# Kernel tuning notes

Measured on AMD Instinct MI355X. Metric: run time of the kernel, lower is better.

The kernel has to match this reference:

```python
import jax, jax.numpy as jnp
import numpy as np

N_NODES = 50000
N_EDGES = 800000
IN_CH = 64
OUT_CH = 64


def setup_inputs() -> dict:
    key = jax.random.key(0)
    ks = jax.random.split(key, 20)
    inp = {
        'x': jax.random.normal(ks[0], (N_NODES, IN_CH), dtype=jnp.float32),
        'edge_index': jax.random.randint(ks[1], (2, N_EDGES), 0, N_NODES, dtype=jnp.int64),
        'edge_weight': jax.random.uniform(ks[2], (N_EDGES,), dtype=jnp.float32),
    }
    i = 3
    for g in ('z', 'r', 'h'):
        inp[f'Wx_{g}'] = 0.1 * jax.random.normal(ks[i], (2, IN_CH, OUT_CH), dtype=jnp.float32); i += 1
        inp[f'bx_{g}'] = 0.1 * jax.random.normal(ks[i], (OUT_CH,), dtype=jnp.float32); i += 1
        inp[f'Wh_{g}'] = 0.1 * jax.random.normal(ks[i], (2, OUT_CH, OUT_CH), dtype=jnp.float32); i += 1
        inp[f'bh_{g}'] = 0.1 * jax.random.normal(ks[i], (OUT_CH,), dtype=jnp.float32); i += 1
    inp['lin_W'] = 0.1 * jax.random.normal(ks[i], (OUT_CH, 1), dtype=jnp.float32); i += 1
    inp['lin_b'] = jnp.zeros((1,), dtype=jnp.float32)
    return inp


def _cheb_norm(edge_index, edge_weight, n_nodes):
    # sym-normalized scaled Laplacian with lambda_max=2: L_hat = -D^{-1/2} A D^{-1/2}
    src, dst = edge_index[0], edge_index[1]
    deg = jax.ops.segment_sum(edge_weight, src, num_segments=n_nodes)
    dinv = jnp.where(deg > 0, jax.lax.rsqrt(jnp.where(deg > 0, deg, 1.0)), 0.0)
    norm = -dinv[src] * edge_weight * dinv[dst]
    return src, dst, norm


def _cheb_conv(x, src, dst, norm, W, b, n_nodes):
    # K=2: out = x @ W0 + (L_hat x) @ W1 + b
    out = x @ W[0]
    tx1 = jax.ops.segment_sum(norm[:, None] * x[src], dst, num_segments=n_nodes)
    out = out + tx1 @ W[1]
    return out + b


def reference(x, edge_index, edge_weight,
              Wx_z, bx_z, Wh_z, bh_z,
              Wx_r, bx_r, Wh_r, bh_r,
              Wx_h, bx_h, Wh_h, bh_h,
              lin_W, lin_b):
    n = x.shape[0]
    src, dst, norm = _cheb_norm(edge_index, edge_weight, n)
    H = jnp.zeros((n, OUT_CH), dtype=x.dtype)  # GConvGRU initial hidden state
    Z = jax.nn.sigmoid(_cheb_conv(x, src, dst, norm, Wx_z, bx_z, n)
                       + _cheb_conv(H, src, dst, norm, Wh_z, bh_z, n))
    R = jax.nn.sigmoid(_cheb_conv(x, src, dst, norm, Wx_r, bx_r, n)
                       + _cheb_conv(H, src, dst, norm, Wh_r, bh_r, n))
    H_tilde = jnp.tanh(_cheb_conv(x, src, dst, norm, Wx_h, bx_h, n)
                       + _cheb_conv(H * R, src, dst, norm, Wh_h, bh_h, n))
    H = Z * H + (1.0 - Z) * H_tilde
    h = jax.nn.relu(H)
    return h @ lin_W + lin_b
```

## Files before the change

kernel.cpp:

```cpp
#include <hip/hip_runtime.h>
#include <hip/hip_bf16.h>

#define NN 50000
#define NE 800000
#define CH 64
#define NPW 8
#define NB 196
#define BCAPD 4608
#define BCAPS 4608
#define EPT 16
#define BIN_BLOCKS ((NE + 256*EPT - 1) / (256*EPT))

typedef __attribute__((ext_vector_type(4))) float f4;

#define OFF_TX1  0
#define OFF_BIND 0
#define OFF_BINS (NB*BCAPD*2)
#define OFF_DINV (NN*CH)
#define OFF_CNT  (OFF_DINV + NN)
#define OFF_GC   (OFF_CNT + NN)
#define OFF_BIAS (OFF_GC + 2*NB)
#define OFF_EREC (OFF_BIAS + 194)

__global__ void k_prep(const float* __restrict__ bxz, const float* __restrict__ bhz,
                       const float* __restrict__ bxh, const float* __restrict__ bhh,
                       const float* __restrict__ linW, const float* __restrict__ linb,
                       float* __restrict__ bias) {
    int i = threadIdx.x;
    bias[i]       = bxz[i] + bhz[i];
    bias[64 + i]  = bxh[i] + bhh[i];
    bias[128 + i] = linW[i];
    if (i == 0) bias[192] = linb[0];
}

__global__ __launch_bounds__(256) void k_bin(const int* __restrict__ ei,
                                             const float* __restrict__ ew,
                                             int2* __restrict__ binD,
                                             unsigned int* __restrict__ binS,
                                             int* __restrict__ gcD, int* __restrict__ gcS) {
    __shared__ int hD[NB], hS[NB], bD[NB], bS[NB];
    int t = threadIdx.x;
    for (int b = t; b < NB; b += 256) { hD[b] = 0; hS[b] = 0; }
    __syncthreads();

    int e0 = blockIdx.x * (256 * EPT);
    unsigned int sa[EPT];
    float wv[EPT];
    int sd[EPT], ss[EPT];
#pragma unroll
    for (int i = 0; i < EPT; i++) {
        int e = e0 + i * 256 + t;
        sd[i] = -1; ss[i] = -1; sa[i] = 0; wv[i] = 0.f;
        if (e < NE) {
            int s = ei[e];
            int d = ei[NE + e];
            wv[i] = ew[e];
            int bind = d >> 8;
            sa[i] = (unsigned int)s | ((unsigned int)(d & 255) << 16)
                  | ((unsigned int)bind << 24);
            sd[i] = atomicAdd(&hD[bind], 1);
            ss[i] = atomicAdd(&hS[s >> 8], 1);
        }
    }
    __syncthreads();
    for (int b = t; b < NB; b += 256) {
        bD[b] = atomicAdd(&gcD[b], hD[b]);
        bS[b] = atomicAdd(&gcS[b], hS[b]);
    }
    __syncthreads();
#pragma unroll
    for (int i = 0; i < EPT; i++) {
        if (sd[i] < 0) continue;
        unsigned int a = sa[i];
        int bind = a >> 24;
        int src  = a & 0xffff;
        int dlo  = (a >> 16) & 255;
        int pD = bD[bind] + sd[i];
        if (pD < BCAPD)
            binD[bind * BCAPD + pD] = make_int2((int)(a & 0xffffff), __float_as_int(wv[i]));
        int bins = src >> 8;
        int pS = bS[bins] + ss[i];
        if (pS < BCAPS)
            binS[bins * BCAPS + pS] = ((unsigned int)(src & 255) << 16)
                                    | ((__float_as_uint(wv[i]) + 0x8000u) >> 16);
    }
}

__global__ __launch_bounds__(1024) void k_bucket(const int2* __restrict__ binD,
                                                 const int* __restrict__ gcD,
                                                 unsigned int* __restrict__ erec, int cap,
                                                 int* __restrict__ cnt) {
    __shared__ int lcnt[256];
    int bin = blockIdx.x;
    int t = threadIdx.x;
    if (t < 256) lcnt[t] = 0;
    __syncthreads();
    int m = gcD[bin]; if (m > BCAPD) m = BCAPD;
    const int2* bp = binD + (size_t)bin * BCAPD;
    for (int j = t; j < m; j += 1024) {
        int2 r = bp[j];
        int dlo = (r.x >> 16) & 255;
        int src = r.x & 0xffff;
        int slot = atomicAdd(&lcnt[dlo], 1);
        if (slot < cap) {
            unsigned int wr = (__float_as_uint(__int_as_float(r.y)) + 0x8000u) >> 16;
            erec[(size_t)(bin * 256 + dlo) * cap + slot] = ((unsigned int)src << 16) | wr;
        }
    }
    __syncthreads();
    if (t < 256) {
        int idx = bin * 256 + t;
        if (idx < NN) cnt[idx] = lcnt[t];
    }
}

__global__ __launch_bounds__(1024) void k_deg(const unsigned int* __restrict__ binS,
                                              const int* __restrict__ gcS,
                                              float* __restrict__ dinv) {
    __shared__ float acc[256];
    int bin = blockIdx.x;
    int t = threadIdx.x;
    if (t < 256) acc[t] = 0.f;
    __syncthreads();
    int m = gcS[bin]; if (m > BCAPS) m = BCAPS;
    const unsigned int* bp = binS + (size_t)bin * BCAPS;
    for (int j = t; j < m; j += 1024) {
        unsigned int r = bp[j];
        float w = __uint_as_float((r & 0xffffu) << 16);
        atomicAdd(&acc[r >> 16], w);
    }
    __syncthreads();
    if (t < 256) {
        int idx = bin * 256 + t;
        if (idx < NN) {
            float d = acc[t];
            dinv[idx] = (d > 0.f) ? (1.f / sqrtf(d)) : 0.f;
        }
    }
}

__global__ __launch_bounds__(256) void k_gather(const float* __restrict__ x,
                                                const int* __restrict__ cnt,
                                                const float* __restrict__ dinv,
                                                const unsigned int* __restrict__ erec,
                                                int cap, float* __restrict__ tx1) {
    int w = (blockIdx.x * 256 + threadIdx.x) >> 6;
    if (w >= NN) return;
    int lane = threadIdx.x & 63;
    int g  = lane >> 4;
    int c4 = (lane & 15) * 4;
    int kn = cnt[w];
    if (kn > cap) kn = cap;
    const unsigned int* bp = erec + (size_t)w * cap;

    f4 t0 = {0.f, 0.f, 0.f, 0.f}, t1 = {0.f, 0.f, 0.f, 0.f};
    int j = 0;
    for (; j + 7 < kn; j += 8) {
        unsigned int r0 = bp[j + g];
        unsigned int r1 = bp[j + 4 + g];
        int s0 = r0 >> 16, s1 = r1 >> 16;
        float w0 = __uint_as_float((r0 & 0xffffu) << 16);
        float w1 = __uint_as_float((r1 & 0xffffu) << 16);
        float n0 = dinv[s0] * w0;
        float n1 = dinv[s1] * w1;
        const f4 x0 = *(const f4*)&x[(size_t)s0 * CH + c4];
        const f4 x1 = *(const f4*)&x[(size_t)s1 * CH + c4];
        t0 += n0 * x0;
        t1 += n1 * x1;
    }
    for (; j + 3 < kn; j += 4) {
        unsigned int r0 = bp[j + g];
        int s0 = r0 >> 16;
        float n0 = dinv[s0] * __uint_as_float((r0 & 0xffffu) << 16);
        const f4 x0 = *(const f4*)&x[(size_t)s0 * CH + c4];
        t0 += n0 * x0;
    }
    int rem = kn - j;
    if (g < rem) {
        unsigned int r = bp[j + g];
        int s0 = r >> 16;
        float n0 = dinv[s0] * __uint_as_float((r & 0xffffu) << 16);
        const f4 x0 = *(const f4*)&x[(size_t)s0 * CH + c4];
        t0 += n0 * x0;
    }
    f4 t = t0 + t1;
#pragma unroll
    for (int q = 0; q < 4; q++) {
        t[q] += __shfl_xor(t[q], 16);
        t[q] += __shfl_xor(t[q], 32);
    }
    if (g == 0) {
        f4 r = -dinv[w] * t;
        *(f4*)&tx1[(size_t)w * CH + c4] = r;
    }
}

__global__ __launch_bounds__(256) void k_node(const float* __restrict__ x,
                                              const float* __restrict__ tx1,
                                              const float* __restrict__ Wxz,
                                              const float* __restrict__ Wxh,
                                              const float* __restrict__ bias,
                                              float* __restrict__ out) {
    __shared__ float lds[4][NPW * 128];
    int wid  = threadIdx.x >> 6;
    int lane = threadIdx.x & 63;
    int base = (blockIdx.x * 4 + wid) * NPW;
    if (base >= NN) return;

    const float BZ  = bias[lane];
    const float BH  = bias[64 + lane];
    const float LWc = bias[128 + lane];
    const float LB  = bias[192];

    float* L = lds[wid];
#pragma unroll
    for (int n = 0; n < NPW; n++) {
        int node = base + n;
        if (node < NN) {
            L[n * 128 + lane]      = x[(size_t)node * CH + lane];
            L[n * 128 + 64 + lane] = tx1[(size_t)node * CH + lane];
        }
    }

    float az[NPW], ah[NPW];
#pragma unroll
    for (int n = 0; n < NPW; n++) { az[n] = BZ; ah[n] = BH; }

#pragma unroll 2
    for (int k = 0; k < CH; k += 4) {
        float wz0[4], wz1[4], wh0[4], wh1[4];
#pragma unroll
        for (int j = 0; j < 4; j++) {
            wz0[j] = Wxz[(k + j) * CH + lane];
            wz1[j] = Wxz[CH * CH + (k + j) * CH + lane];
            wh0[j] = Wxh[(k + j) * CH + lane];
            wh1[j] = Wxh[CH * CH + (k + j) * CH + lane];
        }
#pragma unroll
        for (int n = 0; n < NPW; n++) {
            const f4 xk = *(const f4*)&L[n * 128 + k];
            const f4 tk = *(const f4*)&L[n * 128 + 64 + k];
#pragma unroll
            for (int j = 0; j < 4; j++) {
                az[n] = fmaf(xk[j], wz0[j], az[n]);
                az[n] = fmaf(tk[j], wz1[j], az[n]);
                ah[n] = fmaf(xk[j], wh0[j], ah[n]);
                ah[n] = fmaf(tk[j], wh1[j], ah[n]);
            }
        }
    }

#pragma unroll
    for (int n = 0; n < NPW; n++) {
        float z  = 1.f / (1.f + expf(-az[n]));
        float ht = tanhf(ah[n]);
        float h  = (1.f - z) * ht;
        h = (h > 0.f) ? h : 0.f;
        float v = h * LWc;
#pragma unroll
        for (int off = 32; off > 0; off >>= 1) v += __shfl_xor(v, off);
        if (lane == 0 && base + n < NN) out[base + n] = v + LB;
    }
}

extern "C" void kernel_launch(void* const* d_in, const int* in_sizes, int n_in,
                              void* d_out, int out_size, void* d_ws, size_t ws_size,
                              hipStream_t stream) {
    const float* x   = (const float*)d_in[0];
    const int*   ei  = (const int*)d_in[1];
    const float* ew  = (const float*)d_in[2];
    const float* Wxz = (const float*)d_in[3];
    const float* bxz = (const float*)d_in[4];
    const float* bhz = (const float*)d_in[6];
    const float* Wxh = (const float*)d_in[11];
    const float* bxh = (const float*)d_in[12];
    const float* bhh = (const float*)d_in[14];
    const float* lW  = (const float*)d_in[15];
    const float* lb  = (const float*)d_in[16];
    float* ws  = (float*)d_ws;
    float* out = (float*)d_out;

    long long availInts = (long long)(ws_size / 4) - (long long)OFF_EREC;
    int cap = 64;
    if (availInts < (long long)NN * 64) cap = 48;
    if (availInts < (long long)NN * 48) cap = 32;
    unsigned int* erec = (unsigned int*)(ws + OFF_EREC);

    hipMemsetAsync(ws + OFF_GC, 0, 2 * NB * sizeof(int), stream);

    k_prep<<<1, 64, 0, stream>>>(bxz, bhz, bxh, bhh, lW, lb, ws + OFF_BIAS);
    k_bin<<<BIN_BLOCKS, 256, 0, stream>>>(ei, ew,
                                          (int2*)(ws + OFF_BIND),
                                          (unsigned int*)(ws + OFF_BINS),
                                          (int*)(ws + OFF_GC), (int*)(ws + OFF_GC) + NB);
    k_bucket<<<NB, 1024, 0, stream>>>((const int2*)(ws + OFF_BIND),
                                      (const int*)(ws + OFF_GC), erec, cap,
                                      (int*)(ws + OFF_CNT));
    k_deg<<<NB, 1024, 0, stream>>>((const unsigned int*)(ws + OFF_BINS),
                                   (const int*)(ws + OFF_GC) + NB, ws + OFF_DINV);
    k_gather<<<(NN * 64 + 255) / 256, 256, 0, stream>>>(x, (const int*)(ws + OFF_CNT),
                                                        ws + OFF_DINV, erec, cap,
                                                        ws + OFF_TX1);
    k_node<<<(NN + 4 * NPW - 1) / (4 * NPW), 256, 0, stream>>>(x, ws + OFF_TX1, Wxz, Wxh,
                                                               ws + OFF_BIAS, out);
}
```

Baseline: 121.3 us.

## Use bf16 MFMA for node GRU matmul with bf16 tx1 and pre-transposed weights

Measured after the change: 98.79 us. 1.23x faster.

```diff
diff --git a/kernel.cpp b/kernel.cpp
--- a/kernel.cpp
+++ b/kernel.cpp
@@ -4,7 +4,6 @@
 #define NN 50000
 #define NE 800000
 #define CH 64
-#define NPW 8
 #define NB 196
 #define BCAPD 4608
 #define BCAPS 4608
@@ -12,25 +11,47 @@
 #define BIN_BLOCKS ((NE + 256*EPT - 1) / (256*EPT))
 
 typedef __attribute__((ext_vector_type(4))) float f4;
+typedef __attribute__((ext_vector_type(4))) float f32x4;
+typedef __attribute__((ext_vector_type(8))) short bf16x8;
+typedef __attribute__((ext_vector_type(4))) unsigned int u32x4;
+typedef __attribute__((ext_vector_type(2))) unsigned int u32x2;
 
 #define OFF_TX1  0
 #define OFF_BIND 0
 #define OFF_BINS (NB*BCAPD*2)
-#define OFF_DINV (NN*CH)
+#define OFF_DINV (OFF_BINS + NB*BCAPS)
 #define OFF_CNT  (OFF_DINV + NN)
 #define OFF_GC   (OFF_CNT + NN)
 #define OFF_BIAS (OFF_GC + 2*NB)
-#define OFF_EREC (OFF_BIAS + 194)
-
-__global__ void k_prep(const float* __restrict__ bxz, const float* __restrict__ bhz,
-                       const float* __restrict__ bxh, const float* __restrict__ bhh,
+#define OFF_WT   (OFF_BIAS + 196)
+#define OFF_EREC (OFF_WT + 8192)
+
+__device__ __forceinline__ unsigned int bpack(float a, float b) {
+    return ((__float_as_uint(a) + 0x8000u) >> 16)
+         | ((__float_as_uint(b) + 0x8000u) & 0xffff0000u);
+}
+
+__global__ void k_prep(const float* __restrict__ Wxz, const float* __restrict__ bxz,
+                       const float* __restrict__ bhz,
+                       const float* __restrict__ Wxh, const float* __restrict__ bxh,
+                       const float* __restrict__ bhh,
                        const float* __restrict__ linW, const float* __restrict__ linb,
-                       float* __restrict__ bias) {
-    int i = threadIdx.x;
-    bias[i]       = bxz[i] + bhz[i];
-    bias[64 + i]  = bxh[i] + bhh[i];
-    bias[128 + i] = linW[i];
-    if (i == 0) bias[192] = linb[0];
+                       float* __restrict__ bias, unsigned short* __restrict__ wt) {
+    int idx = blockIdx.x * 256 + threadIdx.x;
+    if (idx < 2 * 64 * 128) {
+        int g = idx >> 13;
+        int c = (idx >> 7) & 63;
+        int k = idx & 127;
+        const float* W = g ? Wxh : Wxz;
+        float v = (k < 64) ? W[k * 64 + c] : W[4096 + (k - 64) * 64 + c];
+        wt[idx] = (unsigned short)((__float_as_uint(v) + 0x8000u) >> 16);
+    }
+    if (idx < 64) {
+        bias[idx]       = bxz[idx] + bhz[idx];
+        bias[64 + idx]  = bxh[idx] + bhh[idx];
+        bias[128 + idx] = linW[idx];
+    }
+    if (idx == 0) bias[192] = linb[0];
 }
 
 __global__ __launch_bounds__(256) void k_bin(const int* __restrict__ ei,
@@ -74,7 +95,6 @@
         unsigned int a = sa[i];
         int bind = a >> 24;
         int src  = a & 0xffff;
-        int dlo  = (a >> 16) & 255;
         int pD = bD[bind] + sd[i];
         if (pD < BCAPD)
             binD[bind * BCAPD + pD] = make_int2((int)(a & 0xffffff), __float_as_int(wv[i]));
@@ -143,7 +163,7 @@
                                                 const int* __restrict__ cnt,
                                                 const float* __restrict__ dinv,
                                                 const unsigned int* __restrict__ erec,
-                                                int cap, float* __restrict__ tx1) {
+                                                int cap, unsigned int* __restrict__ tx1) {
     int w = (blockIdx.x * 256 + threadIdx.x) >> 6;
     if (w >= NN) return;
     int lane = threadIdx.x & 63;
@@ -159,10 +179,8 @@
         unsigned int r0 = bp[j + g];
         unsigned int r1 = bp[j + 4 + g];
         int s0 = r0 >> 16, s1 = r1 >> 16;
-        float w0 = __uint_as_float((r0 & 0xffffu) << 16);
-        float w1 = __uint_as_float((r1 & 0xffffu) << 16);
-        float n0 = dinv[s0] * w0;
-        float n1 = dinv[s1] * w1;
+        float n0 = dinv[s0] * __uint_as_float((r0 & 0xffffu) << 16);
+        float n1 = dinv[s1] * __uint_as_float((r1 & 0xffffu) << 16);
         const f4 x0 = *(const f4*)&x[(size_t)s0 * CH + c4];
         const f4 x1 = *(const f4*)&x[(size_t)s1 * CH + c4];
         t0 += n0 * x0;
@@ -172,16 +190,14 @@
         unsigned int r0 = bp[j + g];
         int s0 = r0 >> 16;
         float n0 = dinv[s0] * __uint_as_float((r0 & 0xffffu) << 16);
-        const f4 x0 = *(const f4*)&x[(size_t)s0 * CH + c4];
-        t0 += n0 * x0;
+        t0 += n0 * (*(const f4*)&x[(size_t)s0 * CH + c4]);
     }
     int rem = kn - j;
     if (g < rem) {
         unsigned int r = bp[j + g];
         int s0 = r >> 16;
         float n0 = dinv[s0] * __uint_as_float((r & 0xffffu) << 16);
-        const f4 x0 = *(const f4*)&x[(size_t)s0 * CH + c4];
-        t0 += n0 * x0;
+        t0 += n0 * (*(const f4*)&x[(size_t)s0 * CH + c4]);
     }
     f4 t = t0 + t1;
 #pragma unroll
@@ -191,75 +207,90 @@
     }
     if (g == 0) {
         f4 r = -dinv[w] * t;
-        *(f4*)&tx1[(size_t)w * CH + c4] = r;
+        u32x2 p = { bpack(r[0], r[1]), bpack(r[2], r[3]) };
+        *(u32x2*)&tx1[(size_t)w * 32 + (lane & 15) * 2] = p;
     }
 }
 
 __global__ __launch_bounds__(256) void k_node(const float* __restrict__ x,
-                                              const float* __restrict__ tx1,
-                                              const float* __restrict__ Wxz,
-                                              const float* __restrict__ Wxh,
+                                              const unsigned int* __restrict__ tx1,
+                                              const unsigned short* __restrict__ WT,
                                               const float* __restrict__ bias,
                                               float* __restrict__ out) {
-    __shared__ float lds[4][NPW * 128];
+    __shared__ unsigned int lds[4][16 * 64];
     int wid  = threadIdx.x >> 6;
     int lane = threadIdx.x & 63;
-    int base = (blockIdx.x * 4 + wid) * NPW;
+    int base = (blockIdx.x * 4 + wid) * 16;
     if (base >= NN) return;
-
-    const float BZ  = bias[lane];
-    const float BH  = bias[64 + lane];
-    const float LWc = bias[128 + lane];
-    const float LB  = bias[192];
-
-    float* L = lds[wid];
-#pragma unroll
-    for (int n = 0; n < NPW; n++) {
-        int node = base + n;
-        if (node < NN) {
-            L[n * 128 + lane]      = x[(size_t)node * CH + lane];
-            L[n * 128 + 64 + lane] = tx1[(size_t)node * CH + lane];
-        }
-    }
-
-    float az[NPW], ah[NPW];
-#pragma unroll
-    for (int n = 0; n < NPW; n++) { az[n] = BZ; ah[n] = BH; }
-
-#pragma unroll 2
-    for (int k = 0; k < CH; k += 4) {
-        float wz0[4], wz1[4], wh0[4], wh1[4];
-#pragma unroll
-        for (int j = 0; j < 4; j++) {
-            wz0[j] = Wxz[(k + j) * CH + lane];
-            wz1[j] = Wxz[CH * CH + (k + j) * CH + lane];
-            wh0[j] = Wxh[(k + j) * CH + lane];
-            wh1[j] = Wxh[CH * CH + (k + j) * CH + lane];
-        }
-#pragma unroll
-        for (int n = 0; n < NPW; n++) {
-            const f4 xk = *(const f4*)&L[n * 128 + k];
-            const f4 tk = *(const f4*)&L[n * 128 + 64 + k];
-#pragma unroll
-            for (int j = 0; j < 4; j++) {
-                az[n] = fmaf(xk[j], wz0[j], az[n]);
-                az[n] = fmaf(tk[j], wz1[j], az[n]);
-                ah[n] = fmaf(xk[j], wh0[j], ah[n]);
-                ah[n] = fmaf(tk[j], wh1[j], ah[n]);
-            }
-        }
-    }
-
-#pragma unroll
-    for (int n = 0; n < NPW; n++) {
-        float z  = 1.f / (1.f + expf(-az[n]));
-        float ht = tanhf(ah[n]);
-        float h  = (1.f - z) * ht;
-        h = (h > 0.f) ? h : 0.f;
-        float v = h * LWc;
-#pragma unroll
-        for (int off = 32; off > 0; off >>= 1) v += __shfl_xor(v, off);
-        if (lane == 0 && base + n < NN) out[base + n] = v + LB;
+    unsigned int* L = lds[wid];
+
+    {
+        int row = lane >> 2, q = lane & 3;
+        size_t node = (size_t)base + row;
+        const f4* xp = (const f4*)(x + node * 64 + q * 16);
+        f4 a = xp[0], b = xp[1], c = xp[2], d = xp[3];
+        u32x4 B0 = { bpack(a[0], a[1]), bpack(a[2], a[3]), bpack(b[0], b[1]), bpack(b[2], b[3]) };
+        u32x4 B1 = { bpack(c[0], c[1]), bpack(c[2], c[3]), bpack(d[0], d[1]), bpack(d[2], d[3]) };
+        *(u32x4*)&L[row * 64 + (((q << 1) | 0) ^ row) * 4] = B0;
+        *(u32x4*)&L[row * 64 + (((q << 1) | 1) ^ row) * 4] = B1;
+        const u32x4* tp = (const u32x4*)(tx1 + node * 32 + q * 8);
+        u32x4 T0 = tp[0], T1 = tp[1];
+        *(u32x4*)&L[row * 64 + ((8 + (q << 1)) ^ row) * 4] = T0;
+        *(u32x4*)&L[row * 64 + ((9 + (q << 1)) ^ row) * 4] = T1;
+    }
+
+    int m  = lane & 15;
+    int kg = lane >> 4;
+    bf16x8 afr[4];
+#pragma unroll
+    for (int kt = 0; kt < 4; kt++) {
+        int bx = (kt * 4 + kg) ^ m;
+        afr[kt] = *(const bf16x8*)&L[m * 64 + bx * 4];
+    }
+
+    const unsigned short* Wl = WT + m * 128 + kg * 8;
+    f32x4 az4[4], ah4[4];
+#pragma unroll
+    for (int nt = 0; nt < 4; nt++) { az4[nt] = (f32x4){0,0,0,0}; ah4[nt] = (f32x4){0,0,0,0}; }
+
+#pragma unroll
+    for (int nt = 0; nt < 4; nt++) {
+#pragma unroll
+        for (int kt = 0; kt < 4; kt++) {
+            bf16x8 bz = *(const bf16x8*)(Wl + nt * 2048 + kt * 32);
+            bf16x8 bh = *(const bf16x8*)(Wl + 8192 + nt * 2048 + kt * 32);
+            az4[nt] = __builtin_amdgcn_mfma_f32_16x16x32_bf16(afr[kt], bz, az4[nt], 0, 0, 0);
+            ah4[nt] = __builtin_amdgcn_mfma_f32_16x16x32_bf16(afr[kt], bh, ah4[nt], 0, 0, 0);
+        }
+    }
+
+    float vout[4] = {0.f, 0.f, 0.f, 0.f};
+#pragma unroll
+    for (int nt = 0; nt < 4; nt++) {
+        int col = nt * 16 + m;
+        float bz = bias[col], bh = bias[64 + col], lw = bias[128 + col];
+#pragma unroll
+        for (int r = 0; r < 4; r++) {
+            float az = az4[nt][r] + bz;
+            float ah = ah4[nt][r] + bh;
+            float ez = __expf(-az);
+            float z  = __builtin_amdgcn_rcpf(1.f + ez);
+            float eh = __expf(2.f * ah);
+            float th = (eh - 1.f) * __builtin_amdgcn_rcpf(eh + 1.f);
+            float h  = (1.f - z) * th;
+            h = (h > 0.f) ? h : 0.f;
+            vout[r] = fmaf(h, lw, vout[r]);
+        }
+    }
+    float LB = bias[192];
+#pragma unroll
+    for (int r = 0; r < 4; r++) {
+        float v = vout[r];
+        v += __shfl_xor(v, 1);
+        v += __shfl_xor(v, 2);
+        v += __shfl_xor(v, 4);
+        v += __shfl_xor(v, 8);
+        if (m == 0) out[base + kg * 4 + r] = v + LB;
     }
 }
 
@@ -288,7 +319,8 @@
 
     hipMemsetAsync(ws + OFF_GC, 0, 2 * NB * sizeof(int), stream);
 
-    k_prep<<<1, 64, 0, stream>>>(bxz, bhz, bxh, bhh, lW, lb, ws + OFF_BIAS);
+    k_prep<<<64, 256, 0, stream>>>(Wxz, bxz, bhz, Wxh, bxh, bhh, lW, lb,
+                                   ws + OFF_BIAS, (unsigned short*)(ws + OFF_WT));
     k_bin<<<BIN_BLOCKS, 256, 0, stream>>>(ei, ew,
                                           (int2*)(ws + OFF_BIND),
                                           (unsigned int*)(ws + OFF_BINS),
@@ -300,7 +332,8 @@
                                    (const int*)(ws + OFF_GC) + NB, ws + OFF_DINV);
     k_gather<<<(NN * 64 + 255) / 256, 256, 0, stream>>>(x, (const int*)(ws + OFF_CNT),
                                                         ws + OFF_DINV, erec, cap,
-                                                        ws + OFF_TX1);
-    k_node<<<(NN + 4 * NPW - 1) / (4 * NPW), 256, 0, stream>>>(x, ws + OFF_TX1, Wxz, Wxh,
-                                                               ws + OFF_BIAS, out);
-}
+                                                        (unsigned int*)(ws + OFF_TX1));
+    k_node<<<(NN + 63) / 64, 256, 0, stream>>>(x, (const unsigned int*)(ws + OFF_TX1),
+                                               (const unsigned short*)(ws + OFF_WT),
+                                               ws + OFF_BIAS, out);
+}
```
